# Optimization experiments

Hardware: AMD Instinct MI355X
Metric: run time of the kernel (lower is better)

The kernel has to match this reference:

```python
import jax, jax.numpy as jnp
import numpy as np
from jax import lax

STRIDE, HID, LAT, R, LVL, SCALE = 8, 128, 64, 3, 4, 4
FF = 50 * 60  # frame_flow spatial size


def bilinear_sample(img, x, y):
    # img: [Q,C,H,W]; x,y: [Q,P] float pixel coords; zero outside image. -> [Q,C,P]
    Q, C, H, W = img.shape
    x0 = jnp.floor(x); y0 = jnp.floor(y)
    wx = x - x0; wy = y - y0
    flat = img.reshape(Q, C, H * W)
    def g(ix, iy):
        valid = (ix >= 0) & (ix <= W - 1) & (iy >= 0) & (iy <= H - 1)
        idx = (jnp.clip(iy, 0, H - 1).astype(jnp.int32) * W
               + jnp.clip(ix, 0, W - 1).astype(jnp.int32))[:, None, :]
        v = jnp.take_along_axis(flat, jnp.broadcast_to(idx, (Q, C, x.shape[-1])), axis=2)
        return v * valid[:, None, :]
    return (g(x0, y0) * ((1 - wy) * (1 - wx))[:, None, :]
            + g(x0 + 1, y0) * ((1 - wy) * wx)[:, None, :]
            + g(x0, y0 + 1) * (wy * (1 - wx))[:, None, :]
            + g(x0 + 1, y0 + 1) * (wy * wx)[:, None, :])


def resize_bilinear(img, oh, ow, align_corners):
    # img: [Q,C,H,W] -> [Q,C,oh,ow], matches F.interpolate(mode='bilinear')
    Q, C, H, W = img.shape
    def coords(o, i):
        if align_corners:
            return jnp.linspace(0.0, i - 1.0, o)
        return jnp.clip((jnp.arange(o) + 0.5) * (i / o) - 0.5, 0.0, i - 1.0)
    ys, xs = coords(oh, H), coords(ow, W)
    y0 = jnp.floor(ys).astype(jnp.int32); y1 = jnp.minimum(y0 + 1, H - 1); wy = ys - y0
    x0 = jnp.floor(xs).astype(jnp.int32); x1 = jnp.minimum(x0 + 1, W - 1); wx = xs - x0
    v = jnp.take(img, y0, axis=2) * (1 - wy)[:, None] + jnp.take(img, y1, axis=2) * wy[:, None]
    return jnp.take(v, x0, axis=3) * (1 - wx) + jnp.take(v, x1, axis=3) * wx


def avg_pool2(x):
    return lax.reduce_window(x, 0.0, lax.add, (1, 1, 2, 2), (1, 1, 2, 2), 'VALID') * 0.25


def encode(x, w, stride):
    # patchify conv + instance-norm (surrogate for BasicEncoder, same in/out shapes)
    y = lax.conv_general_dilated(x, w, (stride, stride), 'VALID',
                                 dimension_numbers=('NCHW', 'OIHW', 'NCHW'))
    m = y.mean(axis=(2, 3), keepdims=True)
    v = y.var(axis=(2, 3), keepdims=True)
    return (y - m) * lax.rsqrt(v + 1e-5)


def build_pyramid(fmaps):
    # fmaps: [B,S,C,H,W] -> list of [B*S,C,Hl,Wl] (CorrBlock.__init__)
    B, S, C, H, W = fmaps.shape
    x = fmaps.reshape(B * S, C, H, W)
    pyr = [x]
    for _ in range(LVL - 1):
        x = avg_pool2(x)
        pyr.append(x)
    return pyr


def corr_pyramid(pyr, feats):
    # feats: [B,S,N,C] -> list of [B*S,N,Hl,Wl] (CorrBlock.corr)
    B, S, N, C = feats.shape
    f = feats.reshape(B * S, N, C)
    scale = 1.0 / jnp.sqrt(jnp.float32(C))
    return [jnp.einsum('qnc,qchw->qnhw', f, p) * scale for p in pyr]


def corr_sample(corrs, coords):
    # CorrBlock.sample: bilinear gather of (2R+1)^2 window per level at coords/2^lvl
    B, S, N, _ = coords.shape
    d = jnp.arange(-R, R + 1, dtype=coords.dtype)
    dy, dx = jnp.meshgrid(d, d, indexing='ij')
    dx = dx.reshape(1, -1); dy = dy.reshape(1, -1)
    out = []
    for i, c in enumerate(corrs):
        H, W = c.shape[-2:]
        cen = coords.reshape(B * S * N, 1, 2) / (2.0 ** i)
        x = cen[..., 0] + dx; y = cen[..., 1] + dy  # [BSN,K]
        v = bilinear_sample(c.reshape(B * S * N, 1, H, W), x, y)
        out.append(v.reshape(B, S, N, -1))
    return jnp.concatenate(out, axis=-1)  # [B,S,N,LVL*(2R+1)^2]


def flows_from(coords):
    B, S, N, _ = coords.shape
    f = (coords[:, 1:] - coords[:, :-1]).transpose(0, 2, 1, 3).reshape(B * N, S - 1, 2)
    return jnp.concatenate([f, f[:, -1:]], axis=1)


def delta_block(fc, fl, ff, xy, w1, b1, w2, b2):
    # surrogate for DeltaBlock / DeltaBlock_temp: MLP over concatenated context
    h = jnp.concatenate([fc, fl, ff, xy], axis=-1)
    return jax.nn.relu(h @ w1 + b1) @ w2 + b2  # [B*N,S,2]


def forward_model(rgbs, points_0, fnet_w, fnet_fine_w, linear_w, linear_b,
                  dbs_w1, dbs_b1, dbs_w2, dbs_b2,
                  dbt_w1, dbt_b1, dbt_w2, dbt_b2, iters):
    B, S, C, H, W = rgbs.shape
    N = points_0.shape[1]
    rgbs = 2.0 * (rgbs / 255.0) - 1.0
    rgbs_ = rgbs.reshape(B * S, C, H, W)
    # frame_flow context (assumes B==1, like the torch code): [N,S,3000]
    ff = jnp.concatenate([rgbs_[-1:, 0], rgbs_[1:, 0] - rgbs_[:-1, 0]], axis=0)[:, None]
    ff = resize_bilinear(ff, 50, 60, False).reshape(1, S, FF)
    frame_flow = jnp.broadcast_to(ff, (N, S, FF))

    # ---- initialize_ : coarse stage (stride 8) ----
    Hc, Wc = H // STRIDE, W // STRIDE
    fmaps_c = encode(rgbs_, fnet_w, STRIDE).reshape(B, S, LAT, Hc, Wc)
    coords = jnp.broadcast_to((points_0 / float(STRIDE))[:, None], (B, S, N, 2))
    f0 = bilinear_sample(fmaps_c[:, 0], coords[:, 0, :, 0], coords[:, 0, :, 1]).transpose(0, 2, 1)
    feats = jnp.broadcast_to(f0[:, None], (B, S, N, LAT))
    xys0_c = jnp.broadcast_to(coords[:, 0].transpose(1, 0, 2), (N, S, 2))
    coords = lax.stop_gradient(coords)
    corrs_c = corr_pyramid(build_pyramid(fmaps_c), feats)
    fc = [resize_bilinear(c, 14, 14, True).reshape(B, S, N, 196) for c in corrs_c]
    fcorrs_ = jnp.stack(fc).mean(0).transpose(0, 2, 1, 3).reshape(B * N, S, 196)
    delta = delta_block(fcorrs_, flows_from(coords), frame_flow, xys0_c,
                        dbs_w1, dbs_b1, dbs_w2, dbs_b2)
    coords = coords + delta.reshape(B, N, S, 2).transpose(0, 2, 1, 3)
    coords_init = coords * float(STRIDE)

    # ---- fine refinement (stride 2), iterative ----
    fs = STRIDE // SCALE  # 2
    Hf, Wf = H // fs, W // fs
    fmaps = encode(rgbs_, fnet_fine_w, fs).reshape(B, S, LAT, Hf, Wf)
    coords = coords_init / float(fs)
    pyr = build_pyramid(fmaps)
    f0 = bilinear_sample(fmaps[:, 0], coords[:, 0, :, 0], coords[:, 0, :, 1]).transpose(0, 2, 1)
    corrs1 = corr_pyramid(pyr, jnp.broadcast_to(f0[:, None], (B, S, N, LAT)))
    xys0 = jnp.broadcast_to(coords[:, 0].transpose(1, 0, 2), (N, S, 2))
    inds2 = jnp.clip(jnp.arange(S) - 2, 0, None)
    inds4 = jnp.clip(jnp.arange(S) - 4, 0, None)
    preds = [coords_init]
    for _ in range(iters):
        coords = lax.stop_gradient(coords)
        def shifted_feats(inds, coords=coords):
            fm = fmaps[:, inds].reshape(B * S, LAT, Hf, Wf)
            co = coords[:, inds].reshape(B * S, N, 2)
            return bilinear_sample(fm, co[..., 0], co[..., 1]).transpose(0, 2, 1).reshape(B, S, N, LAT)
        corrs2 = corr_pyramid(pyr, shifted_feats(inds2))
        corrs4 = corr_pyramid(pyr, shifted_feats(inds4))
        def bn(f):
            return f.transpose(0, 2, 1, 3).reshape(B * N, S, -1)
        fcorrs_ = jnp.concatenate([bn(corr_sample(corrs1, coords)),
                                   bn(corr_sample(corrs2, coords)),
                                   bn(corr_sample(corrs4, coords))], axis=2)
        fcorrs_ = fcorrs_ @ linear_w + linear_b  # 588 -> 392
        delta = delta_block(fcorrs_, flows_from(coords), frame_flow, xys0,
                            dbt_w1, dbt_b1, dbt_w2, dbt_b2)
        coords = coords + delta.reshape(B, N, S, 2).transpose(0, 2, 1, 3)
        preds.append(coords * float(fs))
    return jnp.stack(preds)  # [iters+1, B, S, N, 2]


def setup_inputs():
    ks = jax.random.split(jax.random.key(0), 12)
    B, S, N, H, W = 1, 16, 64, 200, 240
    rgbs = jax.random.uniform(ks[0], (B, S, 1, H, W), jnp.float32) * 255.0
    points_0 = jax.random.uniform(ks[1], (B, N, 2), jnp.float32) * jnp.array([W - 1.0, H - 1.0], jnp.float32)
    d_sp, d_tp = 196 + 2 + FF + 2, 392 + 2 + FF + 2
    return {
        'rgbs': rgbs, 'points_0': points_0,
        'fnet_w': jax.random.normal(ks[2], (LAT, 1, STRIDE, STRIDE), jnp.float32) * 0.1,
        'fnet_fine_w': jax.random.normal(ks[3], (LAT, 1, 2, 2), jnp.float32) * 0.3,
        'linear_w': jax.random.normal(ks[4], (588, 392), jnp.float32) / np.sqrt(588.0).astype(np.float32),
        'linear_b': jnp.zeros((392,), jnp.float32),
        'dbs_w1': jax.random.normal(ks[5], (d_sp, HID), jnp.float32) / np.float32(np.sqrt(d_sp)),
        'dbs_b1': jnp.zeros((HID,), jnp.float32),
        'dbs_w2': jax.random.normal(ks[6], (HID, 2), jnp.float32) / np.float32(np.sqrt(HID)),
        'dbs_b2': jnp.zeros((2,), jnp.float32),
        'dbt_w1': jax.random.normal(ks[7], (d_tp, HID), jnp.float32) / np.float32(np.sqrt(d_tp)),
        'dbt_b1': jnp.zeros((HID,), jnp.float32),
        'dbt_w2': jax.random.normal(ks[8], (HID, 2), jnp.float32) / np.float32(np.sqrt(HID)),
        'dbt_b2': jnp.zeros((2,), jnp.float32),
        'iters': 4,
    }


def reference(rgbs, points_0, fnet_w, fnet_fine_w, linear_w, linear_b,
              dbs_w1, dbs_b1, dbs_w2, dbs_b2,
              dbt_w1, dbt_b1, dbt_w2, dbt_b2, iters):
    return forward_model(rgbs, points_0, fnet_w, fnet_fine_w, linear_w, linear_b,
                         dbs_w1, dbs_b1, dbs_w2, dbs_b2,
                         dbt_w1, dbt_b1, dbt_w2, dbt_b2, iters)
```

## Files before the change

### kernel.cpp

```cpp
#include <hip/hip_runtime.h>

constexpr int cS = 16, cN = 64, cH = 200, cW = 240;
constexpr int cHC = 25, cWC = 30;
constexpr int cHF = 100, cWF = 120;
constexpr int cC = 64;
constexpr int cITERS = 4;
constexpr int cNCH = 50, cCHUNK = 60;

typedef _Float16 half8 __attribute__((ext_vector_type(8)));

__device__ __forceinline__ float bilin_hwc(const float* __restrict__ fm, int Hh, int Ww,
                                           float x, float y, int c) {
  x = fminf(fmaxf(x, -2.0e6f), 2.0e6f);
  y = fminf(fmaxf(y, -2.0e6f), 2.0e6f);
  float x0f = floorf(x), y0f = floorf(y);
  int ix = (int)x0f, iy = (int)y0f;
  float wx = x - x0f, wy = y - y0f;
  float acc = 0.f;
  bool vx0 = (ix >= 0) && (ix < Ww), vx1 = (ix + 1 >= 0) && (ix + 1 < Ww);
  bool vy0 = (iy >= 0) && (iy < Hh), vy1 = (iy + 1 >= 0) && (iy + 1 < Hh);
  if (vy0 && vx0) acc += fm[(iy * Ww + ix) * cC + c] * (1.f - wy) * (1.f - wx);
  if (vy0 && vx1) acc += fm[(iy * Ww + ix + 1) * cC + c] * (1.f - wy) * wx;
  if (vy1 && vx0) acc += fm[((iy + 1) * Ww + ix) * cC + c] * wy * (1.f - wx);
  if (vy1 && vx1) acc += fm[((iy + 1) * Ww + ix + 1) * cC + c] * wy * wx;
  return acc;
}

__device__ __forceinline__ float bilin_raw_h(const _Float16* __restrict__ fm, int Hh, int Ww,
                                             float x, float y, int c, float& wsum) {
  x = fminf(fmaxf(x, -2.0e6f), 2.0e6f);
  y = fminf(fmaxf(y, -2.0e6f), 2.0e6f);
  float x0f = floorf(x), y0f = floorf(y);
  int ix = (int)x0f, iy = (int)y0f;
  float wx = x - x0f, wy = y - y0f;
  float acc = 0.f; wsum = 0.f;
  bool vx0 = (ix >= 0) && (ix < Ww), vx1 = (ix + 1 >= 0) && (ix + 1 < Ww);
  bool vy0 = (iy >= 0) && (iy < Hh), vy1 = (iy + 1 >= 0) && (iy + 1 < Hh);
  float w00 = (1.f - wy) * (1.f - wx), w01 = (1.f - wy) * wx;
  float w10 = wy * (1.f - wx), w11 = wy * wx;
  if (vy0 && vx0) { acc += (float)fm[(iy * Ww + ix) * cC + c] * w00; wsum += w00; }
  if (vy0 && vx1) { acc += (float)fm[(iy * Ww + ix + 1) * cC + c] * w01; wsum += w01; }
  if (vy1 && vx0) { acc += (float)fm[((iy + 1) * Ww + ix) * cC + c] * w10; wsum += w10; }
  if (vy1 && vx1) { acc += (float)fm[((iy + 1) * Ww + ix + 1) * cC + c] * w11; wsum += w11; }
  return acc;
}

constexpr int NB_FFP = 800, NB_CONVC = 1024, NB_CONVF = 1600;

__global__ __launch_bounds__(256) void k_front(const float* __restrict__ rgbs,
                                               const float* __restrict__ w1s,
                                               const float* __restrict__ w1t,
                                               const float* __restrict__ fnw,
                                               const float* __restrict__ fnfw,
                                               float* __restrict__ part,
                                               float* __restrict__ fmc,
                                               _Float16* __restrict__ fmf,
                                               float* __restrict__ partf) {
  __shared__ float smem[512];
  int bid = blockIdx.x, tid = threadIdx.x;
  const float a = 2.0f / 255.0f;

  if (bid < NB_FFP) {
    int s = bid / cNCH, ch = bid % cNCH;
    if (tid < cCHUNK) {
      const float* cur = rgbs + (size_t)s * cH * cW;
      const float* prev = rgbs + (size_t)(s - 1) * cH * cW;
      const float* last = rgbs + (size_t)15 * cH * cW;
      int y = 4 * ch + 1, x = 4 * tid + 1;
      float v = 0.f;
      #pragma unroll
      for (int dy = 0; dy < 2; dy++)
        #pragma unroll
        for (int dx = 0; dx < 2; dx++) {
          int id = (y + dy) * cW + (x + dx);
          float pv = (s == 0) ? (a * last[id] - 1.0f) : (a * (cur[id] - prev[id]));
          v += pv;
        }
      smem[tid] = 0.25f * v;
    }
    __syncthreads();
    int t = tid >> 7, j = tid & 127;
    const float* w = (t == 0) ? (w1s + (size_t)198 * 128) : (w1t + (size_t)394 * 128);
    const float* wr = w + (size_t)ch * cCHUNK * 128 + j;
    float acc = 0.f;
    #pragma unroll 4
    for (int i = 0; i < cCHUNK; i++) acc += smem[i] * wr[(size_t)i * 128];
    part[(((size_t)t * cS + s) * cNCH + ch) * 128 + j] = acc;

  } else if (bid < NB_FFP + NB_CONVC) {
    int idx = bid - NB_FFP;
    int q = idx >> 6, c = idx & 63;
    float* wl = smem;
    float* red = smem + 64;
    if (tid < 64) wl[tid] = fnw[c * 64 + tid];
    __syncthreads();
    const float* img = rgbs + (size_t)q * cH * cW;
    float vals[3];
    float sum = 0.f, ss = 0.f;
    #pragma unroll
    for (int i = 0; i < 3; i++) {
      int pos = tid + i * 256;
      float v = 0.f;
      if (pos < 750) {
        int y = pos / cWC, x = pos % cWC;
        const float* base = img + (y * 8) * cW + x * 8;
        float acc = 0.f, wsum = 0.f;
        for (int ky = 0; ky < 8; ky++)
          #pragma unroll
          for (int kx = 0; kx < 8; kx++) {
            float wv = wl[ky * 8 + kx];
            acc += wv * base[ky * cW + kx];
            wsum += wv;
          }
        v = a * acc - wsum;
        sum += v; ss += v * v;
      }
      vals[i] = v;
    }
    red[tid] = sum; __syncthreads();
    for (int st = 128; st > 0; st >>= 1) { if (tid < st) red[tid] += red[tid + st]; __syncthreads(); }
    float tsum = red[0]; __syncthreads();
    red[tid] = ss; __syncthreads();
    for (int st = 128; st > 0; st >>= 1) { if (tid < st) red[tid] += red[tid + st]; __syncthreads(); }
    float tss = red[0];
    float mean = tsum / 750.0f;
    float var = tss / 750.0f - mean * mean;
    float rstd = rsqrtf(var + 1e-5f);
    #pragma unroll
    for (int i = 0; i < 3; i++) {
      int pos = tid + i * 256;
      if (pos < 750) fmc[((size_t)q * 750 + pos) * cC + c] = (vals[i] - mean) * rstd;
    }

  } else {
    int idx = bid - NB_FFP - NB_CONVC;
    int q = idx / cHF, y = idx % cHF;
    int lane = tid & 63, wv = tid >> 6;
    float w0 = fnfw[lane * 4 + 0], w1 = fnfw[lane * 4 + 1];
    float w2 = fnfw[lane * 4 + 2], w3 = fnfw[lane * 4 + 3];
    float wsum = w0 + w1 + w2 + w3;
    const float* img = rgbs + (size_t)q * cH * cW;
    float sum = 0.f, ss = 0.f;
    for (int x = wv; x < cWF; x += 4) {
      const float* b = img + (2 * y) * cW + 2 * x;
      float v = a * (w0 * b[0] + w1 * b[1] + w2 * b[cW] + w3 * b[cW + 1]) - wsum;
      fmf[(((size_t)q * cHF + y) * cWF + x) * cC + lane] = (_Float16)v;
      sum += v; ss += v * v;
    }
    float* red = smem;
    red[(0 * 4 + wv) * 64 + lane] = sum;
    red[(1 * 4 + wv) * 64 + lane] = ss;
    __syncthreads();
    if (wv == 0) {
      float s4 = red[0 * 64 + lane] + red[1 * 64 + lane] + red[2 * 64 + lane] + red[3 * 64 + lane];
      float q4 = red[(4 + 0) * 64 + lane] + red[(4 + 1) * 64 + lane] +
                 red[(4 + 2) * 64 + lane] + red[(4 + 3) * 64 + lane];
      size_t o = ((size_t)q * cHF + y) * 64 + lane;
      partf[o * 2 + 0] = s4;
      partf[o * 2 + 1] = q4;
    }
  }
}

__global__ __launch_bounds__(256) void k_mid(const float* __restrict__ part,
                                             float* __restrict__ ffw_s, float* __restrict__ ffw_t,
                                             const float* __restrict__ lw, const float* __restrict__ lb,
                                             const float* __restrict__ w1t, const float* __restrict__ b1t,
                                             _Float16* __restrict__ LWc, float* __restrict__ b1te,
                                             const float* __restrict__ partf, float* __restrict__ stats,
                                             const float* __restrict__ fmc, float* __restrict__ arp) {
  __shared__ float smem[14784];
  int bid = blockIdx.x, tid = threadIdx.x;

  if (bid < 16) {
    int s = bid, t = tid >> 7, j = tid & 127;
    const float* p = part + (((size_t)t * cS + s) * cNCH) * 128 + j;
    float acc = 0.f;
    for (int c = 0; c < cNCH; c++) acc += p[(size_t)c * 128];
    ((t == 0) ? ffw_s : ffw_t)[s * 128 + j] = acc;

  } else if (bid < 91) {
    int b2 = bid - 16, g = tid >> 7, j = tid & 127;
    if (b2 < 74) {
      int k0 = b2 * 8 + g * 4;
      if (k0 < 588) {
        const float* l0 = lw + (size_t)(k0 + 0) * 392;
        const float* l1 = lw + (size_t)(k0 + 1) * 392;
        const float* l2 = lw + (size_t)(k0 + 2) * 392;
        const float* l3 = lw + (size_t)(k0 + 3) * 392;
        float a0 = 0.f, a1 = 0.f, a2 = 0.f, a3 = 0.f;
        for (int m = 0; m < 392; m++) {
          float wv = w1t[(size_t)m * 128 + j];
          a0 += l0[m] * wv; a1 += l1[m] * wv; a2 += l2[m] * wv; a3 += l3[m] * wv;
        }
        LWc[(size_t)(k0 + 0) * 128 + j] = (_Float16)a0;
        LWc[(size_t)(k0 + 1) * 128 + j] = (_Float16)a1;
        LWc[(size_t)(k0 + 2) * 128 + j] = (_Float16)a2;
        LWc[(size_t)(k0 + 3) * 128 + j] = (_Float16)a3;
      }
    } else if (g == 0) {
      float acc = b1t[j];
      for (int m = 0; m < 392; m++) acc += lb[m] * w1t[(size_t)m * 128 + j];
      b1te[j] = acc;
    }

  } else if (bid < 107) {
    int q = bid - 91, c = tid & 63, g = tid >> 6;
    float s0 = 0.f, s1 = 0.f;
    for (int yy = 0; yy < 25; yy++) {
      size_t o = ((size_t)q * cHF + g * 25 + yy) * 64 + c;
      s0 += partf[o * 2 + 0];
      s1 += partf[o * 2 + 1];
    }
    smem[g * 64 + c] = s0;
    smem[256 + g * 64 + c] = s1;
    __syncthreads();
    if (g == 0) {
      stats[(q * 64 + c) * 2 + 0] = smem[c] + smem[64 + c] + smem[128 + c] + smem[192 + c];
      stats[(q * 64 + c) * 2 + 1] = smem[256 + c] + smem[320 + c] + smem[384 + c] + smem[448 + c];
    }

  } else {
    int q = bid - 107;
    float* pc1 = smem;
    float* pc2 = smem + 11520;
    float* pc3 = smem + 14208;
    const float* L0 = fmc + (size_t)q * 750 * cC;
    for (int i = tid; i < 12 * 15 * 64; i += 256) {
      int c = i & 63, pos = i >> 6, oy = pos / 15, ox = pos % 15;
      const float* b = L0 + ((2 * oy) * 30 + 2 * ox) * cC + c;
      pc1[i] = 0.25f * (b[0] + b[cC] + b[30 * cC] + b[30 * cC + cC]);
    }
    __syncthreads();
    for (int i = tid; i < 6 * 7 * 64; i += 256) {
      int c = i & 63, pos = i >> 6, oy = pos / 7, ox = pos % 7;
      const float* b = pc1 + ((2 * oy) * 15 + 2 * ox) * cC + c;
      pc2[i] = 0.25f * (b[0] + b[cC] + b[15 * cC] + b[15 * cC + cC]);
    }
    __syncthreads();
    for (int i = tid; i < 3 * 3 * 64; i += 256) {
      int c = i & 63, pos = i >> 6, oy = pos / 3, ox = pos % 3;
      const float* b = pc2 + ((2 * oy) * 7 + 2 * ox) * cC + c;
      pc3[i] = 0.25f * (b[0] + b[cC] + b[7 * cC] + b[7 * cC + cC]);
    }
    __syncthreads();
    const int Hs[4] = {25, 12, 6, 3}, Ws[4] = {30, 15, 7, 3};
    for (int i = tid; i < 196 * 64; i += 256) {
      int c = i & 63, pos = i >> 6, o = pos / 14, p = pos % 14;
      float acc = 0.f;
      #pragma unroll
      for (int l = 0; l < 4; l++) {
        float yy = (float)(o * (Hs[l] - 1)) / 13.0f;
        float xx = (float)(p * (Ws[l] - 1)) / 13.0f;
        int y0 = (int)floorf(yy); int y1 = min(y0 + 1, Hs[l] - 1); float wy = yy - (float)y0;
        int x0 = (int)floorf(xx); int x1 = min(x0 + 1, Ws[l] - 1); float wx = xx - (float)x0;
        const float* L = (l == 0) ? L0 : ((l == 1) ? pc1 : ((l == 2) ? pc2 : pc3));
        float v00 = L[(y0 * Ws[l] + x0) * cC + c], v01 = L[(y0 * Ws[l] + x1) * cC + c];
        float v10 = L[(y1 * Ws[l] + x0) * cC + c], v11 = L[(y1 * Ws[l] + x1) * cC + c];
        acc += (v00 * (1.f - wy) + v10 * wy) * (1.f - wx) + (v01 * (1.f - wy) + v11 * wy) * wx;
      }
      arp[((size_t)q * 196 + pos) * cC + c] = acc * 0.25f * 0.125f;
    }
  }
}

__global__ __launch_bounds__(128) void k_mlp_coarse(const float* __restrict__ arp, const float* __restrict__ fmc,
                                                    const float* __restrict__ w1, const float* __restrict__ b1,
                                                    const float* __restrict__ ffw, const float* __restrict__ w2,
                                                    const float* __restrict__ b2,
                                                    const float* __restrict__ pts, float* __restrict__ cof,
                                                    float* __restrict__ out) {
  int n = blockIdx.x >> 2, sb = (blockIdx.x & 3) * 4;
  __shared__ float fc[4][196];
  __shared__ float f0l[64];
  __shared__ float hl[4][128];
  int j = threadIdx.x;
  float xx = pts[n * 2 + 0] * 0.125f, yy = pts[n * 2 + 1] * 0.125f;
  if (j < 64) f0l[j] = bilin_hwc(fmc, cHC, cWC, xx, yy, j);
  __syncthreads();
  #pragma unroll
  for (int r = 0; r < 4; r++) {
    int s = sb + r;
    for (int k = j; k < 196; k += 128) {
      const float4* b4 = (const float4*)(arp + ((size_t)s * 196 + k) * cC);
      float acc = 0.f;
      #pragma unroll
      for (int c4 = 0; c4 < 16; c4++) {
        float4 v = b4[c4];
        acc += v.x * f0l[c4 * 4 + 0] + v.y * f0l[c4 * 4 + 1] +
               v.z * f0l[c4 * 4 + 2] + v.w * f0l[c4 * 4 + 3];
      }
      fc[r][k] = acc;
    }
  }
  __syncthreads();
  float h0 = 0.f, h1 = 0.f, h2 = 0.f, h3 = 0.f;
  for (int k = 0; k < 196; k++) {
    float wv = w1[(size_t)k * 128 + j];
    h0 += fc[0][k] * wv; h1 += fc[1][k] * wv; h2 += fc[2][k] * wv; h3 += fc[3][k] * wv;
  }
  float hh[4] = {h0, h1, h2, h3};
  const float* Wxy = w1 + (size_t)3198 * 128;
  #pragma unroll
  for (int r = 0; r < 4; r++) {
    int s = sb + r;
    float v = hh[r] + b1[j] + ffw[s * 128 + j] + xx * Wxy[j] + yy * Wxy[128 + j];
    hl[r][j] = fmaxf(v, 0.f);
  }
  __syncthreads();
  if (j < 8) {
    int r = j >> 1, d = j & 1;
    float acc = b2[d];
    for (int k = 0; k < 128; k++) acc += hl[r][k] * w2[k * 2 + d];
    int s = sb + r;
    float base = pts[n * 2 + d] * 0.125f;
    float cc = base + acc;
    out[((size_t)s * cN + n) * 2 + d] = cc * 8.0f;
    cof[((size_t)s * cN + n) * 2 + d] = cc * 4.0f;
  }
}

__global__ __launch_bounds__(256) void k_pyrf(const _Float16* __restrict__ fmf,
                                              _Float16* __restrict__ pf1,
                                              _Float16* __restrict__ pf2,
                                              _Float16* __restrict__ pf3,
                                              const float* __restrict__ stats,
                                              const float* __restrict__ cof,
                                              float* __restrict__ f0f,
                                              float* __restrict__ xys) {
  int q = blockIdx.x, b = blockIdx.y, tid = threadIdx.x;
  if (b == 13) {
    int n = q * 4 + (tid >> 6), c = tid & 63;
    float x = cof[n * 2 + 0], y = cof[n * 2 + 1];
    float ws;
    float raw = bilin_raw_h(fmf, cHF, cWF, x, y, c, ws);
    float su = stats[c * 2 + 0], qq = stats[c * 2 + 1];
    float mean = su / 12000.f, var = qq / 12000.f - mean * mean;
    float rstd = rsqrtf(var + 1e-5f);
    f0f[n * cC + c] = (raw - mean * ws) * rstd;
    if (c < 2) xys[n * 2 + c] = (c == 0) ? x : y;
    return;
  }
  __shared__ _Float16 l1[4 * 60 * 64];
  __shared__ _Float16 l2[2 * 30 * 64];
  int nr1 = (b == 12) ? 2 : 4;
  const _Float16* F = fmf + (size_t)q * cHF * cWF * cC;
  for (int i = tid; i < nr1 * 60 * 64; i += 256) {
    int c = i & 63, pos = i >> 6, rl = pos / 60, ox = pos % 60;
    int r1 = 4 * b + rl;
    const _Float16* p = F + ((size_t)(2 * r1) * cWF + 2 * ox) * cC + c;
    float v = 0.25f * ((float)p[0] + (float)p[cC] + (float)p[cWF * cC] + (float)p[cWF * cC + cC]);
    _Float16 h = (_Float16)v;
    l1[i] = h;
    pf1[(((size_t)q * 50 + r1) * 60 + ox) * cC + c] = h;
  }
  __syncthreads();
  int nr2 = (b == 12) ? 1 : 2;
  for (int i = tid; i < nr2 * 30 * 64; i += 256) {
    int c = i & 63, pos = i >> 6, rl = pos / 30, ox = pos % 30;
    const _Float16* p = l1 + ((2 * rl) * 60 + 2 * ox) * 64 + c;
    float v = 0.25f * ((float)p[0] + (float)p[64] + (float)p[60 * 64] + (float)p[60 * 64 + 64]);
    _Float16 h = (_Float16)v;
    l2[i] = h;
    pf2[(((size_t)q * 25 + 2 * b + rl) * 30 + ox) * cC + c] = h;
  }
  __syncthreads();
  if (b < 12) {
    for (int i = tid; i < 15 * 64; i += 256) {
      int c = i & 63, ox = i >> 6;
      const _Float16* p = l2 + (2 * ox) * 64 + c;
      float v = 0.25f * ((float)p[0] + (float)p[64] + (float)p[30 * 64] + (float)p[30 * 64 + 64]);
      pf3[(((size_t)q * 12 + b) * 15 + ox) * cC + c] = (_Float16)v;
    }
  }
}

__global__ __launch_bounds__(256) void k_iter(const _Float16* __restrict__ p0, const _Float16* __restrict__ p1,
                                              const _Float16* __restrict__ p2, const _Float16* __restrict__ p3,
                                              const float* __restrict__ f0, const float* __restrict__ stats,
                                              const _Float16* __restrict__ LWc, const float* __restrict__ b1e,
                                              const float* __restrict__ ffw, const float* __restrict__ w1t,
                                              const float* __restrict__ w2, const float* __restrict__ b2,
                                              const float* __restrict__ cof_cur, float* __restrict__ cof_nxt,
                                              const float* __restrict__ xys, float* __restrict__ out) {
  int bid = blockIdx.x;
  int w = (bid & 7) * 128 + (bid >> 3);
  int s = w >> 6, n = w & 63;
  __shared__ float feat2[3][64];
  __shared__ float biasS[3];
  __shared__ float fcL[588];
  __shared__ float hp[2][128];
  __shared__ float hl[128];
  int tid = threadIdx.x;

  {
    int t = tid >> 6, c = tid & 63;
    if (t < 3) {
      float sS = stats[(s * 64 + c) * 2 + 0], qS = stats[(s * 64 + c) * 2 + 1];
      float meanS = sS / 12000.f, varS = qS / 12000.f - meanS * meanS;
      float rstdS = rsqrtf(varS + 1e-5f);
      float featn;
      if (t == 0) {
        featn = f0[(size_t)n * cC + c];
      } else {
        int ssrc = max(s - 2 * t, 0);
        float s2 = stats[(ssrc * 64 + c) * 2 + 0], q2 = stats[(ssrc * 64 + c) * 2 + 1];
        float m2 = s2 / 12000.f, v2 = q2 / 12000.f - m2 * m2;
        float r2 = rsqrtf(v2 + 1e-5f);
        float fx = cof_cur[((size_t)ssrc * cN + n) * 2 + 0];
        float fy = cof_cur[((size_t)ssrc * cN + n) * 2 + 1];
        float ws;
        float raw = bilin_raw_h(p0 + (size_t)ssrc * cHF * cWF * cC, cHF, cWF, fx, fy, c, ws);
        featn = (raw - m2 * ws) * r2;
      }
      feat2[t][c] = featn * rstdS * 0.125f;
      float bc = featn * (-meanS * rstdS) * 0.125f;
      #pragma unroll
      for (int o = 32; o; o >>= 1) bc += __shfl_xor(bc, o);
      if (c == 0) biasS[t] = bc;
    }
  }
  __syncthreads();

  {
    int l = tid >> 6, lane = tid & 63;
    const _Float16* Ls[4] = {p0, p1, p2, p3};
    const int Hs[4] = {cHF, 50, 25, 12}, Ws[4] = {cWF, 60, 30, 15};
    float cx = cof_cur[((size_t)s * cN + n) * 2 + 0];
    float cy = cof_cur[((size_t)s * cN + n) * 2 + 1];
    float sc = 1.0f / (float)(1 << l);
    float x = fminf(fmaxf(cx * sc, -2.0e6f), 2.0e6f);
    float y = fminf(fmaxf(cy * sc, -2.0e6f), 2.0e6f);
    float x0f = floorf(x), y0f = floorf(y);
    float wx = x - x0f, wy = y - y0f;
    int dxi = lane & 7, dyi = lane >> 3;
    int ix = (int)x0f + dxi - 3, iy = (int)y0f + dyi - 3;
    int Hl = Hs[l], Wl = Ws[l];
    float d[3] = {0.f, 0.f, 0.f};
    if (ix >= 0 && ix < Wl && iy >= 0 && iy < Hl) {
      const _Float16* row = Ls[l] + (((size_t)s * Hl + iy) * Wl + ix) * cC;
      float a0 = 0.f, a1 = 0.f, a2 = 0.f;
      #pragma unroll
      for (int c8 = 0; c8 < 8; c8++) {
        half8 v = *(const half8*)(row + c8 * 8);
        #pragma unroll
        for (int e = 0; e < 8; e++) {
          float f = (float)v[e];
          a0 += f * feat2[0][c8 * 8 + e];
          a1 += f * feat2[1][c8 * 8 + e];
          a2 += f * feat2[2][c8 * 8 + e];
        }
      }
      d[0] = a0 + biasS[0]; d[1] = a1 + biasS[1]; d[2] = a2 + biasS[2];
    }
    int dy = lane / 7, dx = lane - dy * 7;
    int bb = (lane < 49) ? (dy * 8 + dx) : 0;
    float w00 = (1.f - wy) * (1.f - wx), w01 = (1.f - wy) * wx;
    float w10 = wy * (1.f - wx), w11 = wy * wx;
    #pragma unroll
    for (int t = 0; t < 3; t++) {
      float d00 = __shfl(d[t], bb, 64);
      float d01 = __shfl(d[t], bb + 1, 64);
      float d10 = __shfl(d[t], bb + 8, 64);
      float d11 = __shfl(d[t], bb + 9, 64);
      if (lane < 49)
        fcL[t * 196 + l * 49 + lane] = w00 * d00 + w01 * d01 + w10 * d10 + w11 * d11;
    }
  }
  __syncthreads();

  int j = tid & 127, half = tid >> 7;
  {
    float h = 0.f;
    int k0 = half * 294;
    const _Float16* Lw = LWc + (size_t)k0 * 128 + j;
    for (int k = 0; k < 294; k++) h += fcL[k0 + k] * (float)Lw[(size_t)k * 128];
    hp[half][j] = h;
  }
  __syncthreads();
  if (half == 0) {
    const float* Wfl = w1t + (size_t)392 * 128;
    const float* Wxy = w1t + (size_t)3394 * 128;
    float xx = xys[n * 2 + 0], yy = xys[n * 2 + 1];
    int sA = min(s + 1, 15), sB = (s == 15) ? 14 : s;
    float flx = cof_cur[(sA * cN + n) * 2 + 0] - cof_cur[(sB * cN + n) * 2 + 0];
    float fly = cof_cur[(sA * cN + n) * 2 + 1] - cof_cur[(sB * cN + n) * 2 + 1];
    float v = hp[0][j] + hp[1][j] + b1e[j] + ffw[s * 128 + j] +
              flx * Wfl[j] + fly * Wfl[128 + j] + xx * Wxy[j] + yy * Wxy[128 + j];
    hl[j] = fmaxf(v, 0.f);
  }
  __syncthreads();
  if (tid < 2) {
    int d = tid;
    float acc = b2[d];
    for (int k = 0; k < 128; k++) acc += hl[k] * w2[k * 2 + d];
    float cc = cof_cur[((size_t)s * cN + n) * 2 + d] + acc;
    cof_nxt[((size_t)s * cN + n) * 2 + d] = cc;
    out[((size_t)s * cN + n) * 2 + d] = cc * 2.0f;
  }
}

extern "C" void kernel_launch(void* const* d_in, const int* in_sizes, int n_in,
                              void* d_out, int out_size, void* d_ws, size_t ws_size,
                              hipStream_t stream) {
  (void)in_sizes; (void)n_in; (void)out_size; (void)ws_size;
  const float* rgbs = (const float*)d_in[0];
  const float* pts  = (const float*)d_in[1];
  const float* fnw  = (const float*)d_in[2];
  const float* fnfw = (const float*)d_in[3];
  const float* lw   = (const float*)d_in[4];
  const float* lb   = (const float*)d_in[5];
  const float* w1s  = (const float*)d_in[6];
  const float* b1s  = (const float*)d_in[7];
  const float* w2s  = (const float*)d_in[8];
  const float* b2s  = (const float*)d_in[9];
  const float* w1t  = (const float*)d_in[10];
  const float* b1t  = (const float*)d_in[11];
  const float* w2t  = (const float*)d_in[12];
  const float* b2t  = (const float*)d_in[13];
  float* out = (float*)d_out;

  float* p = (float*)d_ws;
  auto alloc = [&](size_t nf) { float* r = p; p += nf; return r; };
  float* part  = alloc((size_t)2 * cS * cNCH * 128);
  float* ffw_s = alloc(cS * 128);
  float* ffw_t = alloc(cS * 128);
  _Float16* LWc = (_Float16*)alloc((size_t)588 * 128 / 2);
  float* b1te  = alloc(128);
  float* fmc   = alloc((size_t)cS * cHC * cWC * cC);
  float* arp   = alloc((size_t)cS * 196 * cC);
  float* partf = alloc((size_t)cS * cHF * cC * 2);
  float* stats = alloc(cS * cC * 2);
  _Float16* fmf = (_Float16*)alloc((size_t)cS * cHF * cWF * cC / 2);
  _Float16* pf1 = (_Float16*)alloc((size_t)cS * 50 * 60 * cC / 2);
  _Float16* pf2 = (_Float16*)alloc((size_t)cS * 25 * 30 * cC / 2);
  _Float16* pf3 = (_Float16*)alloc((size_t)cS * 12 * 15 * cC / 2);
  float* f0f   = alloc((size_t)cN * cC);
  float* xys0  = alloc(cN * 2);
  float* cofA  = alloc((size_t)cS * cN * 2);
  float* cofB  = alloc((size_t)cS * cN * 2);

  k_front<<<NB_FFP + NB_CONVC + NB_CONVF, 256, 0, stream>>>(
      rgbs, w1s, w1t, fnw, fnfw, part, fmc, fmf, partf);
  k_mid<<<123, 256, 0, stream>>>(part, ffw_s, ffw_t, lw, lb, w1t, b1t, LWc, b1te,
                                 partf, stats, fmc, arp);
  k_mlp_coarse<<<256, 128, 0, stream>>>(arp, fmc, w1s, b1s, ffw_s, w2s, b2s, pts, cofA, out);
  k_pyrf<<<dim3(16, 14), 256, 0, stream>>>(fmf, pf1, pf2, pf3, stats, cofA, f0f, xys0);
  float* cbuf[2] = {cofA, cofB};
  for (int it = 0; it < cITERS; it++) {
    float* cur = cbuf[it & 1];
    float* nxt = cbuf[(it & 1) ^ 1];
    k_iter<<<1024, 256, 0, stream>>>(fmf, pf1, pf2, pf3, f0f, stats, LWc, b1te, ffw_t,
                                     w1t, w2t, b2t, cur, nxt, xys0,
                                     out + (size_t)(it + 1) * cS * cN * 2);
  }
}
```

Baseline: 192.9 us.

## Merge coarse MLP and fine pyramid kernels into one launch, recompute f0 in iter

Fuses the coarse MLP kernel and the fine pyramid-building kernel into a single heterogeneous launch. The MLP blocks now use 256 threads and split the hidden-layer reduction across two halves. The separate f0 feature sampling stage is removed, and each k_iter block recomputes the frame-0 feature by bilinear sampling from the fine map at the stored query coordinates. This saves one launch and a serial dependency, at the cost of extra redundant sampling work inside every iteration kernel.

```diff
diff --git a/kernel.cpp b/kernel.cpp
--- a/kernel.cpp
+++ b/kernel.cpp
@@ -8,6 +8,7 @@
 constexpr int cNCH = 50, cCHUNK = 60;
 
 typedef _Float16 half8 __attribute__((ext_vector_type(8)));
+
 
 __device__ __forceinline__ float bilin_hwc(const float* __restrict__ fm, int Hh, int Ww,
                                            float x, float y, int c) {
@@ -264,25 +265,30 @@
   }
 }
 
-__global__ __launch_bounds__(128) void k_mlp_coarse(const float* __restrict__ arp, const float* __restrict__ fmc,
-                                                    const float* __restrict__ w1, const float* __restrict__ b1,
-                                                    const float* __restrict__ ffw, const float* __restrict__ w2,
-                                                    const float* __restrict__ b2,
-                                                    const float* __restrict__ pts, float* __restrict__ cof,
-                                                    float* __restrict__ out) {
-  int n = blockIdx.x >> 2, sb = (blockIdx.x & 3) * 4;
-  __shared__ float fc[4][196];
-  __shared__ float f0l[64];
-  __shared__ float hl[4][128];
-  int j = threadIdx.x;
-  float xx = pts[n * 2 + 0] * 0.125f, yy = pts[n * 2 + 1] * 0.125f;
-  if (j < 64) f0l[j] = bilin_hwc(fmc, cHC, cWC, xx, yy, j);
-  __syncthreads();
-  #pragma unroll
-  for (int r = 0; r < 4; r++) {
-    int s = sb + r;
-    for (int k = j; k < 196; k += 128) {
-      const float4* b4 = (const float4*)(arp + ((size_t)s * 196 + k) * cC);
+__global__ __launch_bounds__(256) void k_mix(const float* __restrict__ arp, const float* __restrict__ fmc,
+                                             const float* __restrict__ w1, const float* __restrict__ b1,
+                                             const float* __restrict__ ffw, const float* __restrict__ w2,
+                                             const float* __restrict__ b2, const float* __restrict__ pts,
+                                             float* __restrict__ cof, float* __restrict__ xys,
+                                             float* __restrict__ out,
+                                             const _Float16* __restrict__ fmf,
+                                             _Float16* __restrict__ pf1, _Float16* __restrict__ pf2,
+                                             _Float16* __restrict__ pf3) {
+  __shared__ __align__(16) unsigned char smemraw[38400];
+  int bid = blockIdx.x, tid = threadIdx.x;
+
+  if (bid < 256) {
+    int n = bid >> 2, sb = (bid & 3) * 4;
+    float* fc = (float*)smemraw;
+    float* f0l = fc + 784;
+    float* hp = f0l + 64;
+    float* hl = hp + 1024;
+    float xx = pts[n * 2 + 0] * 0.125f, yy = pts[n * 2 + 1] * 0.125f;
+    if (tid < 64) f0l[tid] = bilin_hwc(fmc, cHC, cWC, xx, yy, tid);
+    __syncthreads();
+    for (int i = tid; i < 784; i += 256) {
+      int r = i / 196, k = i - r * 196;
+      const float4* b4 = (const float4*)(arp + ((size_t)(sb + r) * 196 + k) * cC);
       float acc = 0.f;
       #pragma unroll
       for (int c4 = 0; c4 < 16; c4++) {
@@ -290,94 +296,83 @@
         acc += v.x * f0l[c4 * 4 + 0] + v.y * f0l[c4 * 4 + 1] +
                v.z * f0l[c4 * 4 + 2] + v.w * f0l[c4 * 4 + 3];
       }
-      fc[r][k] = acc;
-    }
-  }
-  __syncthreads();
-  float h0 = 0.f, h1 = 0.f, h2 = 0.f, h3 = 0.f;
-  for (int k = 0; k < 196; k++) {
-    float wv = w1[(size_t)k * 128 + j];
-    h0 += fc[0][k] * wv; h1 += fc[1][k] * wv; h2 += fc[2][k] * wv; h3 += fc[3][k] * wv;
-  }
-  float hh[4] = {h0, h1, h2, h3};
-  const float* Wxy = w1 + (size_t)3198 * 128;
-  #pragma unroll
-  for (int r = 0; r < 4; r++) {
-    int s = sb + r;
-    float v = hh[r] + b1[j] + ffw[s * 128 + j] + xx * Wxy[j] + yy * Wxy[128 + j];
-    hl[r][j] = fmaxf(v, 0.f);
-  }
-  __syncthreads();
-  if (j < 8) {
-    int r = j >> 1, d = j & 1;
-    float acc = b2[d];
-    for (int k = 0; k < 128; k++) acc += hl[r][k] * w2[k * 2 + d];
-    int s = sb + r;
-    float base = pts[n * 2 + d] * 0.125f;
-    float cc = base + acc;
-    out[((size_t)s * cN + n) * 2 + d] = cc * 8.0f;
-    cof[((size_t)s * cN + n) * 2 + d] = cc * 4.0f;
-  }
-}
-
-__global__ __launch_bounds__(256) void k_pyrf(const _Float16* __restrict__ fmf,
-                                              _Float16* __restrict__ pf1,
-                                              _Float16* __restrict__ pf2,
-                                              _Float16* __restrict__ pf3,
-                                              const float* __restrict__ stats,
-                                              const float* __restrict__ cof,
-                                              float* __restrict__ f0f,
-                                              float* __restrict__ xys) {
-  int q = blockIdx.x, b = blockIdx.y, tid = threadIdx.x;
-  if (b == 13) {
-    int n = q * 4 + (tid >> 6), c = tid & 63;
-    float x = cof[n * 2 + 0], y = cof[n * 2 + 1];
-    float ws;
-    float raw = bilin_raw_h(fmf, cHF, cWF, x, y, c, ws);
-    float su = stats[c * 2 + 0], qq = stats[c * 2 + 1];
-    float mean = su / 12000.f, var = qq / 12000.f - mean * mean;
-    float rstd = rsqrtf(var + 1e-5f);
-    f0f[n * cC + c] = (raw - mean * ws) * rstd;
-    if (c < 2) xys[n * 2 + c] = (c == 0) ? x : y;
-    return;
-  }
-  __shared__ _Float16 l1[4 * 60 * 64];
-  __shared__ _Float16 l2[2 * 30 * 64];
-  int nr1 = (b == 12) ? 2 : 4;
-  const _Float16* F = fmf + (size_t)q * cHF * cWF * cC;
-  for (int i = tid; i < nr1 * 60 * 64; i += 256) {
-    int c = i & 63, pos = i >> 6, rl = pos / 60, ox = pos % 60;
-    int r1 = 4 * b + rl;
-    const _Float16* p = F + ((size_t)(2 * r1) * cWF + 2 * ox) * cC + c;
-    float v = 0.25f * ((float)p[0] + (float)p[cC] + (float)p[cWF * cC] + (float)p[cWF * cC + cC]);
-    _Float16 h = (_Float16)v;
-    l1[i] = h;
-    pf1[(((size_t)q * 50 + r1) * 60 + ox) * cC + c] = h;
-  }
-  __syncthreads();
-  int nr2 = (b == 12) ? 1 : 2;
-  for (int i = tid; i < nr2 * 30 * 64; i += 256) {
-    int c = i & 63, pos = i >> 6, rl = pos / 30, ox = pos % 30;
-    const _Float16* p = l1 + ((2 * rl) * 60 + 2 * ox) * 64 + c;
-    float v = 0.25f * ((float)p[0] + (float)p[64] + (float)p[60 * 64] + (float)p[60 * 64 + 64]);
-    _Float16 h = (_Float16)v;
-    l2[i] = h;
-    pf2[(((size_t)q * 25 + 2 * b + rl) * 30 + ox) * cC + c] = h;
-  }
-  __syncthreads();
-  if (b < 12) {
-    for (int i = tid; i < 15 * 64; i += 256) {
-      int c = i & 63, ox = i >> 6;
-      const _Float16* p = l2 + (2 * ox) * 64 + c;
-      float v = 0.25f * ((float)p[0] + (float)p[64] + (float)p[30 * 64] + (float)p[30 * 64 + 64]);
-      pf3[(((size_t)q * 12 + b) * 15 + ox) * cC + c] = (_Float16)v;
+      fc[i] = acc;
+    }
+    __syncthreads();
+    int j = tid & 127, half = tid >> 7;
+    float h0 = 0.f, h1 = 0.f, h2 = 0.f, h3 = 0.f;
+    int k0 = half * 98;
+    for (int k = k0; k < k0 + 98; k++) {
+      float wv = w1[(size_t)k * 128 + j];
+      h0 += fc[0 * 196 + k] * wv; h1 += fc[1 * 196 + k] * wv;
+      h2 += fc[2 * 196 + k] * wv; h3 += fc[3 * 196 + k] * wv;
+    }
+    hp[(half * 4 + 0) * 128 + j] = h0; hp[(half * 4 + 1) * 128 + j] = h1;
+    hp[(half * 4 + 2) * 128 + j] = h2; hp[(half * 4 + 3) * 128 + j] = h3;
+    __syncthreads();
+    if (half == 0) {
+      const float* Wxy = w1 + (size_t)3198 * 128;
+      #pragma unroll
+      for (int r = 0; r < 4; r++) {
+        int s = sb + r;
+        float v = hp[r * 128 + j] + hp[(4 + r) * 128 + j] + b1[j] +
+                  ffw[s * 128 + j] + xx * Wxy[j] + yy * Wxy[128 + j];
+        hl[r * 128 + j] = fmaxf(v, 0.f);
+      }
+    }
+    __syncthreads();
+    if (tid < 8) {
+      int r = tid >> 1, d = tid & 1;
+      float acc = b2[d];
+      for (int k = 0; k < 128; k++) acc += hl[r * 128 + k] * w2[k * 2 + d];
+      int s = sb + r;
+      float cc = pts[n * 2 + d] * 0.125f + acc;
+      out[((size_t)s * cN + n) * 2 + d] = cc * 8.0f;
+      cof[((size_t)s * cN + n) * 2 + d] = cc * 4.0f;
+      if (s == 0) xys[n * 2 + d] = cc * 4.0f;
+    }
+
+  } else {
+    int u = bid - 256;
+    int q = u / 13, b = u % 13;
+    _Float16* l1 = (_Float16*)smemraw;
+    _Float16* l2 = l1 + 15360;
+    int nr1 = (b == 12) ? 2 : 4;
+    const _Float16* F = fmf + (size_t)q * cHF * cWF * cC;
+    for (int i = tid; i < nr1 * 60 * 64; i += 256) {
+      int c = i & 63, pos = i >> 6, rl = pos / 60, ox = pos % 60;
+      int r1 = 4 * b + rl;
+      const _Float16* p = F + ((size_t)(2 * r1) * cWF + 2 * ox) * cC + c;
+      float v = 0.25f * ((float)p[0] + (float)p[cC] + (float)p[cWF * cC] + (float)p[cWF * cC + cC]);
+      _Float16 h = (_Float16)v;
+      l1[i] = h;
+      pf1[(((size_t)q * 50 + r1) * 60 + ox) * cC + c] = h;
+    }
+    __syncthreads();
+    int nr2 = (b == 12) ? 1 : 2;
+    for (int i = tid; i < nr2 * 30 * 64; i += 256) {
+      int c = i & 63, pos = i >> 6, rl = pos / 30, ox = pos % 30;
+      const _Float16* p = l1 + ((2 * rl) * 60 + 2 * ox) * 64 + c;
+      float v = 0.25f * ((float)p[0] + (float)p[64] + (float)p[60 * 64] + (float)p[60 * 64 + 64]);
+      _Float16 h = (_Float16)v;
+      l2[i] = h;
+      pf2[(((size_t)q * 25 + 2 * b + rl) * 30 + ox) * cC + c] = h;
+    }
+    __syncthreads();
+    if (b < 12) {
+      for (int i = tid; i < 15 * 64; i += 256) {
+        int c = i & 63, ox = i >> 6;
+        const _Float16* p = l2 + (2 * ox) * 64 + c;
+        float v = 0.25f * ((float)p[0] + (float)p[64] + (float)p[30 * 64] + (float)p[30 * 64 + 64]);
+        pf3[(((size_t)q * 12 + b) * 15 + ox) * cC + c] = (_Float16)v;
+      }
     }
   }
 }
 
 __global__ __launch_bounds__(256) void k_iter(const _Float16* __restrict__ p0, const _Float16* __restrict__ p1,
                                               const _Float16* __restrict__ p2, const _Float16* __restrict__ p3,
-                                              const float* __restrict__ f0, const float* __restrict__ stats,
+                                              const float* __restrict__ stats,
                                               const _Float16* __restrict__ LWc, const float* __restrict__ b1e,
                                               const float* __restrict__ ffw, const float* __restrict__ w1t,
                                               const float* __restrict__ w2, const float* __restrict__ b2,
@@ -399,20 +394,19 @@
       float sS = stats[(s * 64 + c) * 2 + 0], qS = stats[(s * 64 + c) * 2 + 1];
       float meanS = sS / 12000.f, varS = qS / 12000.f - meanS * meanS;
       float rstdS = rsqrtf(varS + 1e-5f);
-      float featn;
-      if (t == 0) {
-        featn = f0[(size_t)n * cC + c];
-      } else {
-        int ssrc = max(s - 2 * t, 0);
-        float s2 = stats[(ssrc * 64 + c) * 2 + 0], q2 = stats[(ssrc * 64 + c) * 2 + 1];
-        float m2 = s2 / 12000.f, v2 = q2 / 12000.f - m2 * m2;
-        float r2 = rsqrtf(v2 + 1e-5f);
-        float fx = cof_cur[((size_t)ssrc * cN + n) * 2 + 0];
-        float fy = cof_cur[((size_t)ssrc * cN + n) * 2 + 1];
-        float ws;
-        float raw = bilin_raw_h(p0 + (size_t)ssrc * cHF * cWF * cC, cHF, cWF, fx, fy, c, ws);
-        featn = (raw - m2 * ws) * r2;
-      }
+      int ssrc = (t == 0) ? 0 : max(s - 2 * t, 0);
+      float fx, fy;
+      if (t == 0) { fx = xys[n * 2 + 0]; fy = xys[n * 2 + 1]; }
+      else {
+        fx = cof_cur[((size_t)ssrc * cN + n) * 2 + 0];
+        fy = cof_cur[((size_t)ssrc * cN + n) * 2 + 1];
+      }
+      float s2 = stats[(ssrc * 64 + c) * 2 + 0], q2 = stats[(ssrc * 64 + c) * 2 + 1];
+      float m2 = s2 / 12000.f, v2 = q2 / 12000.f - m2 * m2;
+      float r2 = rsqrtf(v2 + 1e-5f);
+      float ws;
+      float raw = bilin_raw_h(p0 + (size_t)ssrc * cHF * cWF * cC, cHF, cWF, fx, fy, c, ws);
+      float featn = (raw - m2 * ws) * r2;
       feat2[t][c] = featn * rstdS * 0.125f;
       float bc = featn * (-meanS * rstdS) * 0.125f;
       #pragma unroll
@@ -535,7 +529,6 @@
   _Float16* pf1 = (_Float16*)alloc((size_t)cS * 50 * 60 * cC / 2);
   _Float16* pf2 = (_Float16*)alloc((size_t)cS * 25 * 30 * cC / 2);
   _Float16* pf3 = (_Float16*)alloc((size_t)cS * 12 * 15 * cC / 2);
-  float* f0f   = alloc((size_t)cN * cC);
   float* xys0  = alloc(cN * 2);
   float* cofA  = alloc((size_t)cS * cN * 2);
   float* cofB  = alloc((size_t)cS * cN * 2);
@@ -544,13 +537,13 @@
       rgbs, w1s, w1t, fnw, fnfw, part, fmc, fmf, partf);
   k_mid<<<123, 256, 0, stream>>>(part, ffw_s, ffw_t, lw, lb, w1t, b1t, LWc, b1te,
                                  partf, stats, fmc, arp);
-  k_mlp_coarse<<<256, 128, 0, stream>>>(arp, fmc, w1s, b1s, ffw_s, w2s, b2s, pts, cofA, out);
-  k_pyrf<<<dim3(16, 14), 256, 0, stream>>>(fmf, pf1, pf2, pf3, stats, cofA, f0f, xys0);
+  k_mix<<<464, 256, 0, stream>>>(arp, fmc, w1s, b1s, ffw_s, w2s, b2s, pts,
+                                 cofA, xys0, out, fmf, pf1, pf2, pf3);
   float* cbuf[2] = {cofA, cofB};
   for (int it = 0; it < cITERS; it++) {
     float* cur = cbuf[it & 1];
     float* nxt = cbuf[(it & 1) ^ 1];
-    k_iter<<<1024, 256, 0, stream>>>(fmf, pf1, pf2, pf3, f0f, stats, LWc, b1te, ffw_t,
+    k_iter<<<1024, 256, 0, stream>>>(fmf, pf1, pf2, pf3, stats, LWc, b1te, ffw_t,
                                      w1t, w2t, b2t, cur, nxt, xys0,
                                      out + (size_t)(it + 1) * cS * cN * 2);
   }
```

New measurement: 172.4 us, median of 2. -10.6%, faster.
